# Kernel tuning notes

Measured on AMD Instinct MI355X. Metric: run time of the kernel, lower is better.

## Reference

```python
import jax, jax.numpy as jnp
import numpy as np

C_LIGHT = 3e8
SPATIAL, CROP = 128, 128
BIN_LEN, WALL_SIZE, SAMPLING_COEFF, CYCLES = 0.01, 2.0, 2.0, 5
B, D, T = 1, 2, 96


def waveconvparam(bin_resolution, virtual_wavelength, cycles):
    # Gaussian-windowed virtual cos/sin illumination wave (phasor-field heterodyne).
    s_z = bin_resolution * C_LIGHT
    samples = int(round(cycles * virtual_wavelength / s_z))
    num_cycles = samples * s_z / virtual_wavelength
    sigma = 0.3
    grids_k = np.arange(samples, dtype=np.float64) + 1.0
    sin_wave_k = np.sin(2.0 * np.pi * (num_cycles * grids_k) / samples)
    cos_wave_k = np.cos(2.0 * np.pi * (num_cycles * grids_k) / samples)
    n = np.arange(samples, dtype=np.float64) - (samples - 1) / 2.0
    window = np.exp(-0.5 * (n / (sigma * samples)) ** 2)
    return (cos_wave_k * window).astype(np.float32), (sin_wave_k * window).astype(np.float32)


def definePsf(sptial_grid, temprol_grid, slope):
    # Standard LCT light-cone PSF (O'Toole et al.).
    N, M = sptial_grid, temprol_grid
    x = np.linspace(-1.0, 1.0, 2 * N)
    y = np.linspace(-1.0, 1.0, 2 * N)
    z = np.linspace(0.0, 2.0, 2 * M)
    gz, gy, gx = np.meshgrid(z, y, x, indexing='ij')  # (2M, 2N, 2N)
    psf = np.abs(((4.0 * slope) ** 2) * (gx ** 2 + gy ** 2) - gz)
    psf = (psf == psf.min(axis=0, keepdims=True)).astype(np.float64)
    psf = psf / np.sum(psf[:, N, N])
    psf = psf / np.linalg.norm(psf.ravel())
    psf = np.roll(np.roll(psf, N, axis=1), N, axis=2)
    return psf


def resamplingOperator(M):
    mtx = np.zeros((M * M, M), dtype=np.float64)
    x = np.arange(1, M * M + 1)
    mtx[x - 1, np.ceil(np.sqrt(x)).astype(np.int64) - 1] = 1.0
    mtx = mtx / np.sqrt(x)[:, None]
    mtxi = mtx.T.copy()
    K = int(round(np.log2(M)))
    for _ in range(K):
        mtx = 0.5 * (mtx[0::2] + mtx[1::2])
        mtxi = 0.5 * (mtxi[:, 0::2] + mtxi[:, 1::2])
    return mtx.astype(np.float32), mtxi.astype(np.float32)


def setup_inputs() -> dict:
    key = jax.random.key(0)
    bin_resolution = BIN_LEN / C_LIGHT
    trange = CROP * C_LIGHT * bin_resolution
    width = WALL_SIZE / 2.0
    s_lamda_limit = WALL_SIZE / (SPATIAL - 1)
    virtual_wavelength = SAMPLING_COEFF * (s_lamda_limit * 2.0)
    cosw, sinw = waveconvparam(bin_resolution, virtual_wavelength, CYCLES)
    wave_2xk = np.stack([cosw, sinw], axis=0)[:, ::-1].copy()  # time-reversed, matches module
    psf = definePsf(SPATIAL, CROP, width / trange)
    invpsf = np.conjugate(np.fft.fftn(psf))  # (2*CROP, 2*SPATIAL, 2*SPATIAL)
    mtx, mtxi = resamplingOperator(CROP)
    feat = jax.random.normal(key, (B, D, T, SPATIAL, SPATIAL), dtype=jnp.float32)
    return {
        'feture_bxdxtxhxw': feat,
        'wave_2x1xk': jnp.asarray(wave_2xk[:, None, :], dtype=jnp.float32),
        'mtx_MxM': jnp.asarray(mtx),
        'mtxi_MxM': jnp.asarray(mtxi),
        'invpsf_real': jnp.asarray(np.real(invpsf).astype(np.float32)),
        'invpsf_imag': jnp.asarray(np.imag(invpsf).astype(np.float32)),
        'tbes': jnp.array([16], dtype=jnp.int32),
        'tens': jnp.array([112], dtype=jnp.int32),  # tens = tbes + T, used only via zero-padding
    }


def reference(feture_bxdxtxhxw, wave_2x1xk, mtx_MxM, mtxi_MxM, invpsf_real, invpsf_imag, tbes, tens):
    Bn, Dn, Tn, H, W = feture_bxdxtxhxw.shape
    M = mtx_MxM.shape[0]  # temporal grid (= crop)
    N = H                 # spatial grid
    BD = Bn * Dn

    # --- per-item zero-pad in time to length M (batched, replaces python loop) ---
    def pad_one(x_dthw, tbe):
        z = jnp.zeros((Dn, M, H, W), x_dthw.dtype)
        return jax.lax.dynamic_update_slice(z, x_dthw, (0, tbe, 0, 0))
    data = jax.vmap(pad_one)(feture_bxdxtxhxw, tbes).reshape(BD, M, H, W)

    # --- heterodyne: conv1d along time with reversed cos/sin virtual wave ---
    k = wave_2x1xk.shape[2]
    x = data.transpose(0, 2, 3, 1).reshape(BD * H * W, 1, M)
    y = jax.lax.conv_general_dilated(x, wave_2x1xk, (1,), [(k // 2, k // 2)],
                                     dimension_numbers=('NCH', 'OIH', 'NCH'))
    if k % 2 == 0:
        y = y[:, :, 1:]
    data2 = y.reshape(BD, H, W, 2, M).transpose(3, 0, 4, 1, 2).reshape(2 * BD, M, H, W)

    # --- resampling (LCT warp) ---
    tmp = jnp.einsum('mt,bthw->bmhw', mtx_MxM, data2)

    # --- batched 3D FFT deconvolution with conj(PSF spectrum) ---
    pad = jnp.zeros((2 * BD, 2 * M, 2 * N, 2 * N), tmp.dtype).at[:, :M, :N, :N].set(tmp)
    invpsf = invpsf_real + 1j * invpsf_imag  # complex64, (2M, 2N, 2N)
    vol = jnp.fft.ifftn(jnp.fft.fftn(pad, axes=(1, 2, 3)) * invpsf, axes=(1, 2, 3))[:, :M, :N, :N]

    # --- phasor magnitude: |cos_phasor^2 + sin_phasor^2| combine ---
    sq = vol[:BD] ** 2 + vol[BD:] ** 2  # Re = cr^2-ci^2+sr^2-si^2, Im = 2(cr*ci+sr*si)
    sum_real = jnp.real(sq)
    sum_imag = jnp.imag(sq)
    mag = jnp.sqrt(sum_real ** 2 + sum_imag ** 2)
    sqrt_sum = jnp.sqrt(jax.nn.relu((mag + sum_real) * 0.5))

    # --- inverse resampling ---
    out = jnp.einsum('mt,bthw->bmhw', mtxi_MxM, sqrt_sum)
    return out.reshape(Bn, Dn, M, H, W)
```

## Files before the change

### kernel.cpp

```cpp
#include <hip/hip_runtime.h>
#include <math.h>

typedef float2 c32;

__device__ __forceinline__ c32 cadd(c32 a, c32 b){ return make_float2(a.x+b.x, a.y+b.y); }
__device__ __forceinline__ c32 csub(c32 a, c32 b){ return make_float2(a.x-b.x, a.y-b.y); }
__device__ __forceinline__ c32 cmul(c32 a, c32 b){ return make_float2(fmaf(a.x,b.x,-a.y*b.y), fmaf(a.x,b.y,a.y*b.x)); }
__device__ __forceinline__ c32 cmulc(c32 a, c32 b){ return make_float2(fmaf(a.x,b.x, a.y*b.y), fmaf(a.y,b.x,-a.x*b.y)); }

__device__ __forceinline__ int dr4(int p){
  return ((p&3)<<6) | (((p>>2)&3)<<4) | (((p>>4)&3)<<2) | ((p>>6)&3);
}

template<int S>
__device__ __forceinline__ void dif16(c32 (&z)[16]){
  const float C1=0.92387953251128675613f, S1=0.38268343236508977173f, C2=0.70710678118654752440f;
  const float sg = (float)S;
  const c32 W[8] = { {1.f,0.f},{C1,sg*S1},{C2,sg*C2},{S1,sg*C1},{0.f,sg},{-S1,sg*C1},{-C2,sg*C2},{-C1,sg*S1} };
  #pragma unroll
  for(int j=0;j<8;j++){ c32 a=z[j], b=z[j+8]; z[j]=cadd(a,b); z[j+8]=cmul(csub(a,b), W[j]); }
  #pragma unroll
  for(int blk=0; blk<16; blk+=8){
    #pragma unroll
    for(int j=0;j<4;j++){ c32 a=z[blk+j], b=z[blk+j+4]; z[blk+j]=cadd(a,b); z[blk+j+4]=cmul(csub(a,b), W[2*j]); }
  }
  #pragma unroll
  for(int blk=0; blk<16; blk+=4){
    c32 a=z[blk], b=z[blk+2]; z[blk]=cadd(a,b); z[blk+2]=csub(a,b);
    c32 a1=z[blk+1], b1=z[blk+3]; c32 d=csub(a1,b1);
    z[blk+1]=cadd(a1,b1);
    z[blk+3]= (S<0)? make_float2(d.y,-d.x) : make_float2(-d.y,d.x);
  }
  #pragma unroll
  for(int blk=0; blk<16; blk+=2){ c32 a=z[blk], b=z[blk+1]; z[blk]=cadd(a,b); z[blk+1]=csub(a,b); }
}

__device__ __forceinline__ void dit16(c32 (&z)[16]){
  const float C1=0.92387953251128675613f, S1=0.38268343236508977173f, C2=0.70710678118654752440f;
  const c32 Wc[8] = { {1.f,0.f},{C1,S1},{C2,C2},{S1,C1},{0.f,1.f},{-S1,C1},{-C2,C2},{-C1,S1} };
  #pragma unroll
  for(int p=0;p<16;p+=2){ c32 a=z[p], b=z[p+1]; z[p]=cadd(a,b); z[p+1]=csub(a,b); }
  #pragma unroll
  for(int g=0;g<16;g+=4){
    c32 t=z[g+2]; z[g+2]=csub(z[g],t); z[g]=cadd(z[g],t);
    c32 u=z[g+3]; c32 t1=make_float2(-u.y,u.x); z[g+3]=csub(z[g+1],t1); z[g+1]=cadd(z[g+1],t1);
  }
  #pragma unroll
  for(int g=0;g<16;g+=8){
    #pragma unroll
    for(int j=0;j<4;j++){ c32 t=cmul(z[g+4+j], Wc[2*j]); z[g+4+j]=csub(z[g+j],t); z[g+j]=cadd(z[g+j],t); }
  }
  #pragma unroll
  for(int j=0;j<8;j++){ c32 t=cmul(z[8+j], Wc[j]); z[8+j]=csub(z[j],t); z[j]=cadd(z[j],t); }
}

__device__ __forceinline__ long magAddr(int d, int zz, int y, int x){
  int i = ((zz<<7) + y)*128 + x;
  int plane = i >> 15;
  int rem = i & 32767;
  return ((long)d<<24) + (long)plane*65536 + 32768 + rem;
}

__launch_bounds__(256)
__global__ void k_setup(const float* __restrict__ mtx, const float* __restrict__ wave,
                        const int* __restrict__ tbes, c32* __restrict__ A, c32* __restrict__ T,
                        int K, int P){
  __shared__ double2 w256[256];
  __shared__ double gre[128];
  __shared__ double gim[128];
  int tid=threadIdx.x; int v=blockIdx.x;
  double ang = -6.2831853071795864769252867665590 * (double)tid / 256.0;
  w256[tid]=make_double2(cos(ang), sin(ang));
  if(v==0) T[tid]=make_float2((float)w256[tid].x,(float)w256[tid].y);
  __syncthreads();
  if(tid<128){
    int tbe=tbes[0];
    double sr=0.0, si=0.0;
    for(int t=0;t<128;t++){
      int jj = v + tbe + P - t;
      if(jj>=0 && jj<K){
        double mv=(double)mtx[tid*128+t];
        sr += mv*(double)wave[jj];
        si += mv*(double)wave[K+jj];
      }
    }
    gre[tid]=sr; gim[tid]=si;
  }
  __syncthreads();
  double ar=0.0, ai=0.0;
  int k=tid;
  for(int m=0;m<128;m++){
    double2 f=w256[(k*m)&255];
    ar += f.x*gre[m] - f.y*gim[m];
    ai += f.x*gim[m] + f.y*gre[m];
  }
  A[(long)dr4(k)*96 + v] = make_float2((float)ar,(float)ai);
}

__launch_bounds__(256)
__global__ void k_front(const float* __restrict__ feat, const c32* __restrict__ A, c32* __restrict__ buf){
  __shared__ __align__(16) float Xs[48*128];
  __shared__ __align__(16) c32 As[64*48];
  int tid=threadIdx.x; int b=blockIdx.x;
  int d=b>>9, h=(b>>2)&127, kb=(b&3)*64;
  c32 acc[8][4];
  #pragma unroll
  for(int i=0;i<8;i++){
    #pragma unroll
    for(int j=0;j<4;j++) acc[i][j]=make_float2(0.f,0.f);
  }
  int kg=tid>>5, wg=tid&31;
  for(int vc=0; vc<2; vc++){
    #pragma unroll
    for(int i=0;i<6;i++){
      int idx=tid+i*256;
      int v=idx>>5, w4=idx&31;
      *(float4*)&Xs[v*128 + w4*4] = *(const float4*)&feat[(((long)d*96 + vc*48+v)*128 + h)*128 + w4*4];
    }
    #pragma unroll
    for(int i=0;i<6;i++){
      int idx=tid+i*256;
      int kk=idx/24, rem=idx-kk*24;
      *(float4*)&As[kk*48 + rem*2] = *(const float4*)&A[(long)(kb+kk)*96 + vc*48 + rem*2];
    }
    __syncthreads();
    #pragma unroll 4
    for(int vv=0; vv<48; vv++){
      float4 xv = *(const float4*)&Xs[vv*128 + wg*4];
      #pragma unroll
      for(int i=0;i<8;i++){
        c32 a = As[(kg*8+i)*48 + vv];
        acc[i][0].x = fmaf(a.x, xv.x, acc[i][0].x); acc[i][0].y = fmaf(a.y, xv.x, acc[i][0].y);
        acc[i][1].x = fmaf(a.x, xv.y, acc[i][1].x); acc[i][1].y = fmaf(a.y, xv.y, acc[i][1].y);
        acc[i][2].x = fmaf(a.x, xv.z, acc[i][2].x); acc[i][2].y = fmaf(a.y, xv.z, acc[i][2].y);
        acc[i][3].x = fmaf(a.x, xv.w, acc[i][3].x); acc[i][3].y = fmaf(a.y, xv.w, acc[i][3].y);
      }
    }
    __syncthreads();
  }
  #pragma unroll
  for(int i=0;i<8;i++){
    int k=kb+kg*8+i;
    long o = (((long)d*256 + k)*256 + h)*128 + wg*4;
    *(float4*)&buf[o]   = make_float4(acc[i][0].x,acc[i][0].y,acc[i][1].x,acc[i][1].y);
    *(float4*)&buf[o+2] = make_float4(acc[i][2].x,acc[i][2].y,acc[i][3].x,acc[i][3].y);
  }
}

__launch_bounds__(256)
__global__ void k_ffty(c32* __restrict__ buf, const c32* __restrict__ T){
  __shared__ c32 tile[256*17];
  __shared__ c32 Ts[256];
  int tid=threadIdx.x;
  Ts[tid]=T[tid];
  int b=blockIdx.x;
  int d=b>>11, k=(b>>3)&255, w0=(b&7)*16;
  long base = (((long)d*256 + k)*256)*128 + w0;
  __syncthreads();
  #pragma unroll
  for(int it=0; it<4; it++){
    int idx = tid + it*256; int w = idx&15, j = idx>>4;
    c32 x0 = buf[base + (long)j*128 + w];
    c32 x1 = buf[base + (long)(j+64)*128 + w];
    tile[j*17+w] = cadd(x0,x1);
    c32 y1 = make_float2(x0.x + x1.y, x0.y - x1.x);
    c32 y2 = csub(x0,x1);
    c32 y3 = make_float2(x0.x - x1.y, x0.y + x1.x);
    tile[(j+64)*17+w]  = cmul(y1, Ts[j]);
    tile[(j+128)*17+w] = cmul(y2, Ts[(2*j)&255]);
    tile[(j+192)*17+w] = cmul(y3, Ts[(3*j)&255]);
  }
  __syncthreads();
  #pragma unroll
  for(int s=1;s<4;s++){
    int quarter = 64 >> (2*s);
    int m4 = quarter<<2;
    int sh = 2*s;
    #pragma unroll
    for(int it=0;it<4;it++){
      int idx=tid+it*256; int w=idx&15, bf=idx>>4;
      int g = bf/quarter, j = bf - g*quarter;
      int p0 = g*m4 + j;
      c32 x0=tile[p0*17+w], x1=tile[(p0+quarter)*17+w], x2=tile[(p0+2*quarter)*17+w], x3=tile[(p0+3*quarter)*17+w];
      c32 t0=cadd(x0,x2), t1=csub(x0,x2), t2=cadd(x1,x3), t3=csub(x1,x3);
      c32 y0=cadd(t0,t2);
      c32 y2=csub(t0,t2);
      c32 y1=make_float2(t1.x + t3.y, t1.y - t3.x);
      c32 y3=make_float2(t1.x - t3.y, t1.y + t3.x);
      tile[p0*17+w]=y0;
      tile[(p0+quarter)*17+w]  =cmul(y1, Ts[(j<<sh)&255]);
      tile[(p0+2*quarter)*17+w]=cmul(y2, Ts[((2*j)<<sh)&255]);
      tile[(p0+3*quarter)*17+w]=cmul(y3, Ts[((3*j)<<sh)&255]);
    }
    __syncthreads();
  }
  #pragma unroll
  for(int it=0;it<16;it++){
    int idx=tid+it*256; int w=idx&15, p=idx>>4;
    buf[base + (long)p*128 + w] = tile[p*17+w];
  }
}

__launch_bounds__(256)
__global__ void k_fftx(c32* __restrict__ buf, const float* __restrict__ pre,
                       const float* __restrict__ pim, const c32* __restrict__ T){
  __shared__ float lre[16*272];
  __shared__ float lim[16*272];
  __shared__ c32 Ts[256];
  const int BR[16]={0,8,4,12,2,10,6,14,1,9,5,13,3,11,7,15};
  int tid=threadIdx.x;
  Ts[tid]=T[tid];
  int lane = tid & 63;
  int L = ((tid>>6)<<2) + (lane>>4);
  int n1 = lane & 15;
  int k = blockIdx.x >> 5;
  int q = ((blockIdx.x & 31)<<3) + (L & 7);
  int d = L >> 3;
  long lbase = (((long)d*256 + k)*256 + q)*128;
  int Lb = L*272;
  c32 z[16];
  #pragma unroll
  for(int r=0;r<8;r++) z[r] = buf[lbase + n1 + 16*r];
  #pragma unroll
  for(int r=8;r<16;r++) z[r] = make_float2(0.f,0.f);
  __syncthreads();
  dif16<-1>(z);
  #pragma unroll
  for(int r=1;r<16;r++) z[r] = cmul(z[r], Ts[(n1*BR[r])&255]);
  #pragma unroll
  for(int r=0;r<16;r++){ int o = Lb + BR[r]*17 + n1; lre[o]=z[r].x; lim[o]=z[r].y; }
  __syncthreads();
  #pragma unroll
  for(int c=0;c<16;c++){ int o = Lb + n1*17 + c; z[c]=make_float2(lre[o], lim[o]); }
  dif16<-1>(z);
  long prow = (((long)dr4(k))*256 + dr4(q))*256;
  #pragma unroll
  for(int r=0;r<16;r++){
    int kx = n1 + 16*BR[r];
    c32 h = make_float2(pre[prow+kx], pim[prow+kx]);
    z[r] = cmul(z[r], h);
  }
  dit16(z);
  #pragma unroll
  for(int r=1;r<16;r++) z[r] = cmulc(z[r], Ts[(r*n1)&255]);
  __syncthreads();
  #pragma unroll
  for(int r=0;r<16;r++){ int o = Lb + r*17 + n1; lre[o]=z[r].x; lim[o]=z[r].y; }
  __syncthreads();
  #pragma unroll
  for(int c=0;c<16;c++){ int o = Lb + n1*17 + c; z[c]=make_float2(lre[o], lim[o]); }
  dif16<1>(z);
  const float s = 1.f/256.f;
  #pragma unroll
  for(int r=0;r<16;r+=2){
    int n2 = BR[r];
    buf[lbase + n1 + 16*n2] = make_float2(z[r].x*s, z[r].y*s);
  }
}

__launch_bounds__(256)
__global__ void k_iffty(c32* __restrict__ buf, const c32* __restrict__ T){
  __shared__ c32 tile[256*17];
  __shared__ c32 Ts[256];
  int tid=threadIdx.x;
  Ts[tid]=T[tid];
  int b=blockIdx.x;
  int d=b>>11, k=(b>>3)&255, x0=(b&7)*16;
  long base = (((long)d*256 + k)*256)*128 + x0;
  __syncthreads();
  #pragma unroll
  for(int it=0;it<16;it++){
    int idx=tid+it*256; int w=idx&15, p=idx>>4;
    tile[p*17+w]=buf[base + (long)p*128 + w];
  }
  __syncthreads();
  #pragma unroll
  for(int s=0;s<3;s++){
    int quarter = 1<<(2*s);
    int m4 = quarter<<2;
    int sh = 2*(3-s);
    #pragma unroll
    for(int it=0;it<4;it++){
      int idx=tid+it*256; int w=idx&15, bf=idx>>4;
      int g=bf/quarter, j=bf-g*quarter;
      int p0=g*m4+j;
      c32 t0=tile[p0*17+w];
      c32 t1=cmulc(tile[(p0+quarter)*17+w],   Ts[(j<<sh)&255]);
      c32 t2=cmulc(tile[(p0+2*quarter)*17+w], Ts[((2*j)<<sh)&255]);
      c32 t3=cmulc(tile[(p0+3*quarter)*17+w], Ts[((3*j)<<sh)&255]);
      c32 y0 = make_float2(t0.x+t1.x+t2.x+t3.x, t0.y+t1.y+t2.y+t3.y);
      c32 y1 = make_float2(t0.x - t1.y - t2.x + t3.y, t0.y + t1.x - t2.y - t3.x);
      c32 y2 = make_float2(t0.x - t1.x + t2.x - t3.x, t0.y - t1.y + t2.y - t3.y);
      c32 y3 = make_float2(t0.x + t1.y - t2.x - t3.y, t0.y - t1.x - t2.y + t3.x);
      tile[p0*17+w]=y0; tile[(p0+quarter)*17+w]=y1; tile[(p0+2*quarter)*17+w]=y2; tile[(p0+3*quarter)*17+w]=y3;
    }
    __syncthreads();
  }
  const float sc = 1.f/256.f;
  #pragma unroll
  for(int it=0;it<4;it++){
    int idx=tid+it*256; int w=idx&15, j=idx>>4;
    c32 t0=tile[j*17+w];
    c32 t1=cmulc(tile[(j+64)*17+w],  Ts[j]);
    c32 t2=cmulc(tile[(j+128)*17+w], Ts[(2*j)&255]);
    c32 t3=cmulc(tile[(j+192)*17+w], Ts[(3*j)&255]);
    c32 y0 = make_float2((t0.x+t1.x+t2.x+t3.x)*sc, (t0.y+t1.y+t2.y+t3.y)*sc);
    c32 y1 = make_float2((t0.x - t1.y - t2.x + t3.y)*sc, (t0.y + t1.x - t2.y - t3.x)*sc);
    buf[base + (long)j*128 + w] = y0;
    buf[base + (long)(j+64)*128 + w] = y1;
  }
}

__launch_bounds__(256)
__global__ void k_ifftz(c32* __restrict__ buf, const c32* __restrict__ T){
  __shared__ c32 tile[256*17];
  __shared__ c32 Ts[256];
  float* magp = (float*)buf;
  int tid=threadIdx.x;
  Ts[tid]=T[tid];
  int b=blockIdx.x;
  int d=b>>10, y=(b>>3)&127, x0=(b&7)*16;
  __syncthreads();
  #pragma unroll
  for(int it=0;it<16;it++){
    int idx=tid+it*256; int w=idx&15, p=idx>>4;
    tile[p*17+w]=buf[(((long)d*256 + p)*256 + y)*128 + x0 + w];
  }
  __syncthreads();
  #pragma unroll
  for(int s=0;s<3;s++){
    int quarter = 1<<(2*s);
    int m4 = quarter<<2;
    int sh = 2*(3-s);
    #pragma unroll
    for(int it=0;it<4;it++){
      int idx=tid+it*256; int w=idx&15, bf=idx>>4;
      int g=bf/quarter, j=bf-g*quarter;
      int p0=g*m4+j;
      c32 t0=tile[p0*17+w];
      c32 t1=cmulc(tile[(p0+quarter)*17+w],   Ts[(j<<sh)&255]);
      c32 t2=cmulc(tile[(p0+2*quarter)*17+w], Ts[((2*j)<<sh)&255]);
      c32 t3=cmulc(tile[(p0+3*quarter)*17+w], Ts[((3*j)<<sh)&255]);
      c32 y0 = make_float2(t0.x+t1.x+t2.x+t3.x, t0.y+t1.y+t2.y+t3.y);
      c32 y1 = make_float2(t0.x - t1.y - t2.x + t3.y, t0.y + t1.x - t2.y - t3.x);
      c32 y2 = make_float2(t0.x - t1.x + t2.x - t3.x, t0.y - t1.y + t2.y - t3.y);
      c32 y3 = make_float2(t0.x + t1.y - t2.x - t3.y, t0.y - t1.x - t2.y + t3.x);
      tile[p0*17+w]=y0; tile[(p0+quarter)*17+w]=y1; tile[(p0+2*quarter)*17+w]=y2; tile[(p0+3*quarter)*17+w]=y3;
    }
    __syncthreads();
  }
  const float sc = 1.f/256.f;
  #pragma unroll
  for(int it=0;it<4;it++){
    int idx=tid+it*256; int w=idx&15, j=idx>>4;
    c32 t0=tile[j*17+w];
    c32 t1=cmulc(tile[(j+64)*17+w],  Ts[j]);
    c32 t2=cmulc(tile[(j+128)*17+w], Ts[(2*j)&255]);
    c32 t3=cmulc(tile[(j+192)*17+w], Ts[(3*j)&255]);
    float y0r = t0.x+t1.x+t2.x+t3.x, y0i = t0.y+t1.y+t2.y+t3.y;
    float y1r = t0.x - t1.y - t2.x + t3.y, y1i = t0.y + t1.x - t2.y - t3.x;
    magp[magAddr(d, j,    y, x0+w)] = sqrtf(y0r*y0r + y0i*y0i) * sc;
    magp[magAddr(d, j+64, y, x0+w)] = sqrtf(y1r*y1r + y1i*y1i) * sc;
  }
}

__launch_bounds__(256)
__global__ void k_post(const float* __restrict__ magp, const float* __restrict__ mtxi, float* __restrict__ out){
  __shared__ __align__(16) float magT[128*32];
  __shared__ __align__(16) float mt[128*70];
  int tid=threadIdx.x; int b=blockIdx.x;
  int d=b>>10, y=(b>>3)&127, x0=((b>>1)&3)*32, m0=(b&1)*64;
  #pragma unroll
  for(int it=0;it<16;it++){
    int idx=tid+it*256; int x=idx&31, t=idx>>5;
    magT[t*32+x] = magp[magAddr(d,t,y,x0+x)];
  }
  #pragma unroll
  for(int it=0;it<32;it++){
    int idx=tid+it*256; int mm=idx>>7, t=idx&127;
    mt[t*70+mm] = mtxi[(m0+mm)*128 + t];
  }
  __syncthreads();
  int xg=tid&7, mg=tid>>3;
  float4 a0=make_float4(0.f,0.f,0.f,0.f), a1=a0;
  #pragma unroll 4
  for(int t=0;t<128;t++){
    float2 mv = *(const float2*)&mt[t*70 + mg*2];
    float4 g  = *(const float4*)&magT[t*32 + xg*4];
    a0.x = fmaf(mv.x, g.x, a0.x); a0.y = fmaf(mv.x, g.y, a0.y);
    a0.z = fmaf(mv.x, g.z, a0.z); a0.w = fmaf(mv.x, g.w, a0.w);
    a1.x = fmaf(mv.y, g.x, a1.x); a1.y = fmaf(mv.y, g.y, a1.y);
    a1.z = fmaf(mv.y, g.z, a1.z); a1.w = fmaf(mv.y, g.w, a1.w);
  }
  int m_ = m0 + mg*2;
  *(float4*)&out[(((long)d*128 + m_  )*128 + y)*128 + x0 + xg*4] = a0;
  *(float4*)&out[(((long)d*128 + m_+1)*128 + y)*128 + x0 + xg*4] = a1;
}

extern "C" void kernel_launch(void* const* d_in, const int* in_sizes, int n_in,
                              void* d_out, int out_size, void* d_ws, size_t ws_size,
                              hipStream_t stream) {
  const float* feat=(const float*)d_in[0];
  const float* wave=(const float*)d_in[1];
  const float* mtx =(const float*)d_in[2];
  const float* mtxi=(const float*)d_in[3];
  const float* pre =(const float*)d_in[4];
  const float* pim =(const float*)d_in[5];
  const int*   tbes=(const int*)d_in[6];
  float* out=(float*)d_out;
  char* ws=(char*)d_ws;
  c32* A   = (c32*)ws;
  c32* T   = (c32*)(ws + 196608);
  c32* buf = (c32*)(ws + 262144);

  int K = in_sizes[1] / 2;
  int P = (K & 1) ? (K/2) : (K/2 - 1);

  hipLaunchKernelGGL(k_setup, dim3(96),   dim3(256), 0, stream, mtx, wave, tbes, A, T, K, P);
  hipLaunchKernelGGL(k_front, dim3(1024), dim3(256), 0, stream, feat, A, buf);
  hipLaunchKernelGGL(k_ffty,  dim3(4096), dim3(256), 0, stream, buf, T);
  hipLaunchKernelGGL(k_fftx,  dim3(8192), dim3(256), 0, stream, buf, pre, pim, T);
  hipLaunchKernelGGL(k_iffty, dim3(4096), dim3(256), 0, stream, buf, T);
  hipLaunchKernelGGL(k_ifftz, dim3(2048), dim3(256), 0, stream, buf, T);
  hipLaunchKernelGGL(k_post,  dim3(2048), dim3(256), 0, stream, (const float*)buf, mtxi, out);
}
```

Before: 247.1 us.

## Fuse y-FFT, x-FFT with PSF multiply, and inverse y-FFT into one plane kernel

Three separate kernels (forward y-FFT, x-FFT with PSF multiply and inverse x-FFT, inverse y-FFT) are replaced by one k_plane kernel. Each 1024-thread block holds a whole (d,k) plane in shared memory and runs the 256-point y transform as 16x8x2 stages, with the zero-padded half split into two passes (py). The x transforms do their transpose with warp shuffles instead of LDS round trips. This removes two full global-memory round trips of the large complex buffer and two launches. In exchange, the kernel uses about 132KB of shared memory, runs 512 large blocks with low occupancy, and needs more register pressure and syncthreads.

```diff
diff --git a/kernel.cpp b/kernel.cpp
--- a/kernel.cpp
+++ b/kernel.cpp
@@ -52,6 +52,48 @@
   }
   #pragma unroll
   for(int j=0;j<8;j++){ c32 t=cmul(z[8+j], Wc[j]); z[8+j]=csub(z[j],t); z[j]=cadd(z[j],t); }
+}
+
+template<int S>
+__device__ __forceinline__ void dif8(c32 (&z)[8]){
+  const float C2=0.70710678118654752440f;
+  const float sg=(float)S;
+  const c32 W1=make_float2(C2, sg*C2), W2=make_float2(0.f,sg), W3=make_float2(-C2, sg*C2);
+  {
+    c32 a0=z[0],a1=z[1],a2=z[2],a3=z[3],b0=z[4],b1=z[5],b2=z[6],b3=z[7];
+    z[0]=cadd(a0,b0); z[4]=csub(a0,b0);
+    z[1]=cadd(a1,b1); z[5]=cmul(csub(a1,b1),W1);
+    z[2]=cadd(a2,b2); z[6]=cmul(csub(a2,b2),W2);
+    z[3]=cadd(a3,b3); z[7]=cmul(csub(a3,b3),W3);
+  }
+  #pragma unroll
+  for(int h=0;h<8;h+=4){
+    c32 a0=z[h],a1=z[h+1],b0=z[h+2],b1=z[h+3];
+    z[h]=cadd(a0,b0); z[h+2]=csub(a0,b0);
+    c32 dd=csub(a1,b1); z[h+1]=cadd(a1,b1);
+    z[h+3]= (S<0)? make_float2(dd.y,-dd.x) : make_float2(-dd.y,dd.x);
+  }
+  #pragma unroll
+  for(int p=0;p<8;p+=2){ c32 a=z[p],b=z[p+1]; z[p]=cadd(a,b); z[p+1]=csub(a,b); }
+}
+
+__device__ __forceinline__ void transpose16(c32 (&z)[16], int lane){
+  #pragma unroll
+  for(int bsh=0; bsh<4; bsh++){
+    const int b = 1<<bsh;
+    c32 t[16];
+    #pragma unroll
+    for(int r=0;r<16;r++){
+      t[r].x = __shfl_xor(z[r^b].x, b, 16);
+      t[r].y = __shfl_xor(z[r^b].y, b, 16);
+    }
+    #pragma unroll
+    for(int r=0;r<16;r++){
+      bool keep = ((lane & b) == (r & b));
+      z[r].x = keep ? z[r].x : t[r].x;
+      z[r].y = keep ? z[r].y : t[r].y;
+    }
+  }
 }
 
 __device__ __forceinline__ long magAddr(int d, int zz, int y, int x){
@@ -147,167 +189,137 @@
   }
 }
 
-__launch_bounds__(256)
-__global__ void k_ffty(c32* __restrict__ buf, const c32* __restrict__ T){
-  __shared__ c32 tile[256*17];
-  __shared__ c32 Ts[256];
-  int tid=threadIdx.x;
-  Ts[tid]=T[tid];
-  int b=blockIdx.x;
-  int d=b>>11, k=(b>>3)&255, w0=(b&7)*16;
-  long base = (((long)d*256 + k)*256)*128 + w0;
-  __syncthreads();
-  #pragma unroll
-  for(int it=0; it<4; it++){
-    int idx = tid + it*256; int w = idx&15, j = idx>>4;
-    c32 x0 = buf[base + (long)j*128 + w];
-    c32 x1 = buf[base + (long)(j+64)*128 + w];
-    tile[j*17+w] = cadd(x0,x1);
-    c32 y1 = make_float2(x0.x + x1.y, x0.y - x1.x);
-    c32 y2 = csub(x0,x1);
-    c32 y3 = make_float2(x0.x - x1.y, x0.y + x1.x);
-    tile[(j+64)*17+w]  = cmul(y1, Ts[j]);
-    tile[(j+128)*17+w] = cmul(y2, Ts[(2*j)&255]);
-    tile[(j+192)*17+w] = cmul(y3, Ts[(3*j)&255]);
-  }
-  __syncthreads();
-  #pragma unroll
-  for(int s=1;s<4;s++){
-    int quarter = 64 >> (2*s);
-    int m4 = quarter<<2;
-    int sh = 2*s;
-    #pragma unroll
-    for(int it=0;it<4;it++){
-      int idx=tid+it*256; int w=idx&15, bf=idx>>4;
-      int g = bf/quarter, j = bf - g*quarter;
-      int p0 = g*m4 + j;
-      c32 x0=tile[p0*17+w], x1=tile[(p0+quarter)*17+w], x2=tile[(p0+2*quarter)*17+w], x3=tile[(p0+3*quarter)*17+w];
-      c32 t0=cadd(x0,x2), t1=csub(x0,x2), t2=cadd(x1,x3), t3=csub(x1,x3);
-      c32 y0=cadd(t0,t2);
-      c32 y2=csub(t0,t2);
-      c32 y1=make_float2(t1.x + t3.y, t1.y - t3.x);
-      c32 y3=make_float2(t1.x - t3.y, t1.y + t3.x);
-      tile[p0*17+w]=y0;
-      tile[(p0+quarter)*17+w]  =cmul(y1, Ts[(j<<sh)&255]);
-      tile[(p0+2*quarter)*17+w]=cmul(y2, Ts[((2*j)<<sh)&255]);
-      tile[(p0+3*quarter)*17+w]=cmul(y3, Ts[((3*j)<<sh)&255]);
-    }
-    __syncthreads();
-  }
-  #pragma unroll
-  for(int it=0;it<16;it++){
-    int idx=tid+it*256; int w=idx&15, p=idx>>4;
-    buf[base + (long)p*128 + w] = tile[p*17+w];
-  }
-}
-
-__launch_bounds__(256)
-__global__ void k_fftx(c32* __restrict__ buf, const float* __restrict__ pre,
-                       const float* __restrict__ pim, const c32* __restrict__ T){
-  __shared__ float lre[16*272];
-  __shared__ float lim[16*272];
+#define PSTR 129
+__launch_bounds__(1024)
+__global__ void k_plane(c32* __restrict__ buf, const float* __restrict__ pre,
+                        const float* __restrict__ pim, const c32* __restrict__ T){
+  __shared__ float Pre[128*PSTR];
+  __shared__ float Pim[128*PSTR];
   __shared__ c32 Ts[256];
   const int BR[16]={0,8,4,12,2,10,6,14,1,9,5,13,3,11,7,15};
+  const int BR3[8]={0,4,2,6,1,5,3,7};
   int tid=threadIdx.x;
-  Ts[tid]=T[tid];
-  int lane = tid & 63;
-  int L = ((tid>>6)<<2) + (lane>>4);
-  int n1 = lane & 15;
-  int k = blockIdx.x >> 5;
-  int q = ((blockIdx.x & 31)<<3) + (L & 7);
-  int d = L >> 3;
-  long lbase = (((long)d*256 + k)*256 + q)*128;
-  int Lb = L*272;
-  c32 z[16];
-  #pragma unroll
-  for(int r=0;r<8;r++) z[r] = buf[lbase + n1 + 16*r];
-  #pragma unroll
-  for(int r=8;r<16;r++) z[r] = make_float2(0.f,0.f);
-  __syncthreads();
-  dif16<-1>(z);
-  #pragma unroll
-  for(int r=1;r<16;r++) z[r] = cmul(z[r], Ts[(n1*BR[r])&255]);
-  #pragma unroll
-  for(int r=0;r<16;r++){ int o = Lb + BR[r]*17 + n1; lre[o]=z[r].x; lim[o]=z[r].y; }
-  __syncthreads();
-  #pragma unroll
-  for(int c=0;c<16;c++){ int o = Lb + n1*17 + c; z[c]=make_float2(lre[o], lim[o]); }
-  dif16<-1>(z);
-  long prow = (((long)dr4(k))*256 + dr4(q))*256;
-  #pragma unroll
-  for(int r=0;r<16;r++){
-    int kx = n1 + 16*BR[r];
-    c32 h = make_float2(pre[prow+kx], pim[prow+kx]);
-    z[r] = cmul(z[r], h);
-  }
-  dit16(z);
-  #pragma unroll
-  for(int r=1;r<16;r++) z[r] = cmulc(z[r], Ts[(r*n1)&255]);
-  __syncthreads();
-  #pragma unroll
-  for(int r=0;r<16;r++){ int o = Lb + r*17 + n1; lre[o]=z[r].x; lim[o]=z[r].y; }
-  __syncthreads();
-  #pragma unroll
-  for(int c=0;c<16;c++){ int o = Lb + n1*17 + c; z[c]=make_float2(lre[o], lim[o]); }
-  dif16<1>(z);
-  const float s = 1.f/256.f;
-  #pragma unroll
-  for(int r=0;r<16;r+=2){
-    int n2 = BR[r];
-    buf[lbase + n1 + 16*n2] = make_float2(z[r].x*s, z[r].y*s);
-  }
-}
-
-__launch_bounds__(256)
-__global__ void k_iffty(c32* __restrict__ buf, const c32* __restrict__ T){
-  __shared__ c32 tile[256*17];
-  __shared__ c32 Ts[256];
-  int tid=threadIdx.x;
-  Ts[tid]=T[tid];
-  int b=blockIdx.x;
-  int d=b>>11, k=(b>>3)&255, x0=(b&7)*16;
-  long base = (((long)d*256 + k)*256)*128 + x0;
-  __syncthreads();
-  #pragma unroll
-  for(int it=0;it<16;it++){
-    int idx=tid+it*256; int w=idx&15, p=idx>>4;
-    tile[p*17+w]=buf[base + (long)p*128 + w];
-  }
-  __syncthreads();
-  #pragma unroll
-  for(int s=0;s<3;s++){
-    int quarter = 1<<(2*s);
-    int m4 = quarter<<2;
-    int sh = 2*(3-s);
-    #pragma unroll
-    for(int it=0;it<4;it++){
-      int idx=tid+it*256; int w=idx&15, bf=idx>>4;
-      int g=bf/quarter, j=bf-g*quarter;
-      int p0=g*m4+j;
-      c32 t0=tile[p0*17+w];
-      c32 t1=cmulc(tile[(p0+quarter)*17+w],   Ts[(j<<sh)&255]);
-      c32 t2=cmulc(tile[(p0+2*quarter)*17+w], Ts[((2*j)<<sh)&255]);
-      c32 t3=cmulc(tile[(p0+3*quarter)*17+w], Ts[((3*j)<<sh)&255]);
-      c32 y0 = make_float2(t0.x+t1.x+t2.x+t3.x, t0.y+t1.y+t2.y+t3.y);
-      c32 y1 = make_float2(t0.x - t1.y - t2.x + t3.y, t0.y + t1.x - t2.y - t3.x);
-      c32 y2 = make_float2(t0.x - t1.x + t2.x - t3.x, t0.y - t1.y + t2.y - t3.y);
-      c32 y3 = make_float2(t0.x + t1.y - t2.x - t3.y, t0.y - t1.x - t2.y + t3.x);
-      tile[p0*17+w]=y0; tile[(p0+quarter)*17+w]=y1; tile[(p0+2*quarter)*17+w]=y2; tile[(p0+3*quarter)*17+w]=y3;
-    }
-    __syncthreads();
-  }
-  const float sc = 1.f/256.f;
-  #pragma unroll
-  for(int it=0;it<4;it++){
-    int idx=tid+it*256; int w=idx&15, j=idx>>4;
-    c32 t0=tile[j*17+w];
-    c32 t1=cmulc(tile[(j+64)*17+w],  Ts[j]);
-    c32 t2=cmulc(tile[(j+128)*17+w], Ts[(2*j)&255]);
-    c32 t3=cmulc(tile[(j+192)*17+w], Ts[(3*j)&255]);
-    c32 y0 = make_float2((t0.x+t1.x+t2.x+t3.x)*sc, (t0.y+t1.y+t2.y+t3.y)*sc);
-    c32 y1 = make_float2((t0.x - t1.y - t2.x + t3.y)*sc, (t0.y + t1.x - t2.y - t3.x)*sc);
-    buf[base + (long)j*128 + w] = y0;
-    buf[base + (long)(j+64)*128 + w] = y1;
+  if(tid<256) Ts[tid]=T[tid];
+  int b=blockIdx.x; int d=b>>8, k=b&255;
+  long pbase = (((long)d*256 + k)*256)*128;
+  int g = tid>>7, x = tid&127;
+  int lane16 = tid&15, rowslot = tid>>4;
+  long prowz = ((long)dr4(k))*65536;
+  c32 Oacc[16];
+  #pragma unroll
+  for(int j=0;j<16;j++) Oacc[j]=make_float2(0.f,0.f);
+
+  for(int py=0; py<2; py++){
+    c32 v[16];
+    #pragma unroll
+    for(int j=0;j<16;j++){
+      c32 val = buf[pbase + (long)(g+8*j)*128 + x];
+      if(py){ val = cmul(val, Ts[g+8*j]); }
+      v[j]=val;
+    }
+    __syncthreads();
+    dif16<-1>(v);
+    #pragma unroll
+    for(int r=0;r<16;r++){
+      int k1 = BR[r];
+      c32 val = cmul(v[r], Ts[(2*g*k1)&255]);
+      int row = k1*8+g;
+      Pre[row*PSTR+x]=val.x; Pim[row*PSTR+x]=val.y;
+    }
+    __syncthreads();
+    c32 u0[8], u1[8];
+    #pragma unroll
+    for(int gp=0; gp<8; gp++){
+      int r0=(2*g)*8+gp;
+      u0[gp]=make_float2(Pre[r0*PSTR+x],Pim[r0*PSTR+x]);
+      u1[gp]=make_float2(Pre[(r0+8)*PSTR+x],Pim[(r0+8)*PSTR+x]);
+    }
+    __syncthreads();
+    dif8<-1>(u0); dif8<-1>(u1);
+    #pragma unroll
+    for(int r=0;r<8;r++){
+      int row0=2*g+16*BR3[r];
+      Pre[row0*PSTR+x]=u0[r].x;     Pim[row0*PSTR+x]=u0[r].y;
+      Pre[(row0+1)*PSTR+x]=u1[r].x; Pim[(row0+1)*PSTR+x]=u1[r].y;
+    }
+    __syncthreads();
+    #pragma unroll
+    for(int s=0;s<2;s++){
+      int row = s*64 + rowslot;
+      long prow = prowz + (long)(2*row+py)*256;
+      c32 z[16];
+      #pragma unroll
+      for(int r=0;r<8;r++) z[r]=make_float2(Pre[row*PSTR + lane16 + 16*r], Pim[row*PSTR + lane16 + 16*r]);
+      #pragma unroll
+      for(int r=8;r<16;r++) z[r]=make_float2(0.f,0.f);
+      dif16<-1>(z);
+      #pragma unroll
+      for(int r=1;r<16;r++) z[r]=cmul(z[r], Ts[(lane16*BR[r])&255]);
+      c32 y[16];
+      #pragma unroll
+      for(int a=0;a<16;a++) y[a]=z[BR[a]];
+      transpose16(y, lane16);
+      dif16<-1>(y);
+      #pragma unroll
+      for(int r=0;r<16;r++){
+        int kx = lane16 + 16*BR[r];
+        c32 h = make_float2(pre[prow+kx], pim[prow+kx]);
+        y[r]=cmul(y[r],h);
+      }
+      dit16(y);
+      #pragma unroll
+      for(int r=1;r<16;r++) y[r]=cmulc(y[r], Ts[(r*lane16)&255]);
+      transpose16(y, lane16);
+      dif16<1>(y);
+      const float s256=1.f/256.f;
+      #pragma unroll
+      for(int r=0;r<16;r+=2){
+        int n2=BR[r];
+        Pre[row*PSTR + lane16 + 16*n2] = y[r].x*s256;
+        Pim[row*PSTR + lane16 + 16*n2] = y[r].y*s256;
+      }
+    }
+    __syncthreads();
+    c32 R0[8], R1[8];
+    #pragma unroll
+    for(int k2=0;k2<8;k2++){
+      int row0=2*g+16*k2;
+      R0[k2]=make_float2(Pre[row0*PSTR+x],Pim[row0*PSTR+x]);
+      R1[k2]=make_float2(Pre[(row0+1)*PSTR+x],Pim[(row0+1)*PSTR+x]);
+    }
+    __syncthreads();
+    dif8<1>(R0); dif8<1>(R1);
+    #pragma unroll
+    for(int r=0;r<8;r++){
+      int q8=BR3[r];
+      Pre[(q8*16+2*g)*PSTR+x]=R0[r].x;   Pim[(q8*16+2*g)*PSTR+x]=R0[r].y;
+      Pre[(q8*16+2*g+1)*PSTR+x]=R1[r].x; Pim[(q8*16+2*g+1)*PSTR+x]=R1[r].y;
+    }
+    __syncthreads();
+    c32 w[16];
+    #pragma unroll
+    for(int k1=0;k1<16;k1++){
+      c32 val=make_float2(Pre[(g*16+k1)*PSTR+x],Pim[(g*16+k1)*PSTR+x]);
+      w[k1]=cmulc(val, Ts[(2*g*k1)&255]);
+    }
+    dif16<1>(w);
+    const float sy=1.f/256.f;
+    #pragma unroll
+    for(int j=0;j<16;j++){
+      int q=g+8*j;
+      c32 val=w[BR[j]];
+      if(py==0){
+        Oacc[j].x += val.x*sy; Oacc[j].y += val.y*sy;
+      } else {
+        c32 tw=Ts[q];
+        Oacc[j].x += (val.x*tw.x + val.y*tw.y)*sy;
+        Oacc[j].y += (val.y*tw.x - val.x*tw.y)*sy;
+      }
+    }
+  }
+  #pragma unroll
+  for(int j=0;j<16;j++){
+    buf[pbase + (long)(g+8*j)*128 + x] = Oacc[j];
   }
 }
 
@@ -416,11 +428,9 @@
   int K = in_sizes[1] / 2;
   int P = (K & 1) ? (K/2) : (K/2 - 1);
 
-  hipLaunchKernelGGL(k_setup, dim3(96),   dim3(256), 0, stream, mtx, wave, tbes, A, T, K, P);
-  hipLaunchKernelGGL(k_front, dim3(1024), dim3(256), 0, stream, feat, A, buf);
-  hipLaunchKernelGGL(k_ffty,  dim3(4096), dim3(256), 0, stream, buf, T);
-  hipLaunchKernelGGL(k_fftx,  dim3(8192), dim3(256), 0, stream, buf, pre, pim, T);
-  hipLaunchKernelGGL(k_iffty, dim3(4096), dim3(256), 0, stream, buf, T);
-  hipLaunchKernelGGL(k_ifftz, dim3(2048), dim3(256), 0, stream, buf, T);
-  hipLaunchKernelGGL(k_post,  dim3(2048), dim3(256), 0, stream, (const float*)buf, mtxi, out);
-}
+  hipLaunchKernelGGL(k_setup, dim3(96),   dim3(256),  0, stream, mtx, wave, tbes, A, T, K, P);
+  hipLaunchKernelGGL(k_front, dim3(1024), dim3(256),  0, stream, feat, A, buf);
+  hipLaunchKernelGGL(k_plane, dim3(512),  dim3(1024), 0, stream, buf, pre, pim, T);
+  hipLaunchKernelGGL(k_ifftz, dim3(2048), dim3(256),  0, stream, buf, T);
+  hipLaunchKernelGGL(k_post,  dim3(2048), dim3(256),  0, stream, (const float*)buf, mtxi, out);
+}
```

New measurement: 528.0 us. 114% more time.

## Fuse inverse z-FFT with inverse resampling and use wave barriers in x-FFT

Applied to the files above, without the earlier changes.

Merges the inverse z-FFT and inverse-resampling matmul into one kernel. Each block keeps its 128x16 magnitude tile in shared memory instead of writing it to global memory and reading it back in a separate launch. The x-FFT kernel now uses an interleaved complex shared tile and wave-level barriers in place of block-wide syncs, since each 16-thread group only exchanges data within its own wavefront. The cost is that each block reloads the full mtxi matrix in two halves, and the post stage runs with a narrower per-block x tile.

```diff
diff --git a/kernel.cpp b/kernel.cpp
--- a/kernel.cpp
+++ b/kernel.cpp
@@ -52,13 +52,6 @@
   }
   #pragma unroll
   for(int j=0;j<8;j++){ c32 t=cmul(z[8+j], Wc[j]); z[8+j]=csub(z[j],t); z[j]=cadd(z[j],t); }
-}
-
-__device__ __forceinline__ long magAddr(int d, int zz, int y, int x){
-  int i = ((zz<<7) + y)*128 + x;
-  int plane = i >> 15;
-  int rem = i & 32767;
-  return ((long)d<<24) + (long)plane*65536 + 32768 + rem;
 }
 
 __launch_bounds__(256)
@@ -204,8 +197,7 @@
 __launch_bounds__(256)
 __global__ void k_fftx(c32* __restrict__ buf, const float* __restrict__ pre,
                        const float* __restrict__ pim, const c32* __restrict__ T){
-  __shared__ float lre[16*272];
-  __shared__ float lim[16*272];
+  __shared__ c32 tile[16*276];
   __shared__ c32 Ts[256];
   const int BR[16]={0,8,4,12,2,10,6,14,1,9,5,13,3,11,7,15};
   int tid=threadIdx.x;
@@ -217,7 +209,7 @@
   int q = ((blockIdx.x & 31)<<3) + (L & 7);
   int d = L >> 3;
   long lbase = (((long)d*256 + k)*256 + q)*128;
-  int Lb = L*272;
+  c32* tl = &tile[L*276];
   c32 z[16];
   #pragma unroll
   for(int r=0;r<8;r++) z[r] = buf[lbase + n1 + 16*r];
@@ -228,10 +220,10 @@
   #pragma unroll
   for(int r=1;r<16;r++) z[r] = cmul(z[r], Ts[(n1*BR[r])&255]);
   #pragma unroll
-  for(int r=0;r<16;r++){ int o = Lb + BR[r]*17 + n1; lre[o]=z[r].x; lim[o]=z[r].y; }
-  __syncthreads();
-  #pragma unroll
-  for(int c=0;c<16;c++){ int o = Lb + n1*17 + c; z[c]=make_float2(lre[o], lim[o]); }
+  for(int r=0;r<16;r++) tl[BR[r]*17 + n1] = z[r];
+  __builtin_amdgcn_wave_barrier();
+  #pragma unroll
+  for(int c=0;c<16;c++) z[c] = tl[n1*17 + c];
   dif16<-1>(z);
   long prow = (((long)dr4(k))*256 + dr4(q))*256;
   #pragma unroll
@@ -243,12 +235,12 @@
   dit16(z);
   #pragma unroll
   for(int r=1;r<16;r++) z[r] = cmulc(z[r], Ts[(r*n1)&255]);
-  __syncthreads();
-  #pragma unroll
-  for(int r=0;r<16;r++){ int o = Lb + r*17 + n1; lre[o]=z[r].x; lim[o]=z[r].y; }
-  __syncthreads();
-  #pragma unroll
-  for(int c=0;c<16;c++){ int o = Lb + n1*17 + c; z[c]=make_float2(lre[o], lim[o]); }
+  __builtin_amdgcn_wave_barrier();
+  #pragma unroll
+  for(int r=0;r<16;r++) tl[r*17 + n1] = z[r];
+  __builtin_amdgcn_wave_barrier();
+  #pragma unroll
+  for(int c=0;c<16;c++) z[c] = tl[n1*17 + c];
   dif16<1>(z);
   const float s = 1.f/256.f;
   #pragma unroll
@@ -312,10 +304,11 @@
 }
 
 __launch_bounds__(256)
-__global__ void k_ifftz(c32* __restrict__ buf, const c32* __restrict__ T){
+__global__ void k_back(c32* __restrict__ buf, const float* __restrict__ mtxi,
+                       const c32* __restrict__ T, float* __restrict__ out){
   __shared__ c32 tile[256*17];
+  __shared__ float magl[128*16];
   __shared__ c32 Ts[256];
-  float* magp = (float*)buf;
   int tid=threadIdx.x;
   Ts[tid]=T[tid];
   int b=blockIdx.x;
@@ -359,42 +352,32 @@
     c32 t3=cmulc(tile[(j+192)*17+w], Ts[(3*j)&255]);
     float y0r = t0.x+t1.x+t2.x+t3.x, y0i = t0.y+t1.y+t2.y+t3.y;
     float y1r = t0.x - t1.y - t2.x + t3.y, y1i = t0.y + t1.x - t2.y - t3.x;
-    magp[magAddr(d, j,    y, x0+w)] = sqrtf(y0r*y0r + y0i*y0i) * sc;
-    magp[magAddr(d, j+64, y, x0+w)] = sqrtf(y1r*y1r + y1i*y1i) * sc;
-  }
-}
-
-__launch_bounds__(256)
-__global__ void k_post(const float* __restrict__ magp, const float* __restrict__ mtxi, float* __restrict__ out){
-  __shared__ __align__(16) float magT[128*32];
-  __shared__ __align__(16) float mt[128*70];
-  int tid=threadIdx.x; int b=blockIdx.x;
-  int d=b>>10, y=(b>>3)&127, x0=((b>>1)&3)*32, m0=(b&1)*64;
-  #pragma unroll
-  for(int it=0;it<16;it++){
-    int idx=tid+it*256; int x=idx&31, t=idx>>5;
-    magT[t*32+x] = magp[magAddr(d,t,y,x0+x)];
-  }
-  #pragma unroll
-  for(int it=0;it<32;it++){
-    int idx=tid+it*256; int mm=idx>>7, t=idx&127;
-    mt[t*70+mm] = mtxi[(m0+mm)*128 + t];
-  }
-  __syncthreads();
-  int xg=tid&7, mg=tid>>3;
-  float4 a0=make_float4(0.f,0.f,0.f,0.f), a1=a0;
-  #pragma unroll 4
-  for(int t=0;t<128;t++){
-    float2 mv = *(const float2*)&mt[t*70 + mg*2];
-    float4 g  = *(const float4*)&magT[t*32 + xg*4];
-    a0.x = fmaf(mv.x, g.x, a0.x); a0.y = fmaf(mv.x, g.y, a0.y);
-    a0.z = fmaf(mv.x, g.z, a0.z); a0.w = fmaf(mv.x, g.w, a0.w);
-    a1.x = fmaf(mv.y, g.x, a1.x); a1.y = fmaf(mv.y, g.y, a1.y);
-    a1.z = fmaf(mv.y, g.z, a1.z); a1.w = fmaf(mv.y, g.w, a1.w);
-  }
-  int m_ = m0 + mg*2;
-  *(float4*)&out[(((long)d*128 + m_  )*128 + y)*128 + x0 + xg*4] = a0;
-  *(float4*)&out[(((long)d*128 + m_+1)*128 + y)*128 + x0 + xg*4] = a1;
+    magl[j*16 + w]      = sqrtf(y0r*y0r + y0i*y0i) * sc;
+    magl[(j+64)*16 + w] = sqrtf(y1r*y1r + y1i*y1i) * sc;
+  }
+  __syncthreads();
+  float* mt = (float*)tile;
+  int xg = tid&3, mg = tid>>2;
+  #pragma unroll
+  for(int c=0;c<2;c++){
+    #pragma unroll
+    for(int it=0;it<32;it++){
+      int idx=tid+it*256; int t=idx&127, mm=idx>>7;
+      mt[t*68+mm] = mtxi[(c*64+mm)*128 + t];
+    }
+    __syncthreads();
+    float4 a = make_float4(0.f,0.f,0.f,0.f);
+    #pragma unroll 4
+    for(int t=0;t<128;t++){
+      float mv = mt[t*68 + mg];
+      float4 g = *(const float4*)&magl[t*16 + xg*4];
+      a.x = fmaf(mv, g.x, a.x); a.y = fmaf(mv, g.y, a.y);
+      a.z = fmaf(mv, g.z, a.z); a.w = fmaf(mv, g.w, a.w);
+    }
+    int m_ = c*64 + mg;
+    *(float4*)&out[(((long)d*128 + m_)*128 + y)*128 + x0 + xg*4] = a;
+    __syncthreads();
+  }
 }
 
 extern "C" void kernel_launch(void* const* d_in, const int* in_sizes, int n_in,
@@ -421,6 +404,5 @@
   hipLaunchKernelGGL(k_ffty,  dim3(4096), dim3(256), 0, stream, buf, T);
   hipLaunchKernelGGL(k_fftx,  dim3(8192), dim3(256), 0, stream, buf, pre, pim, T);
   hipLaunchKernelGGL(k_iffty, dim3(4096), dim3(256), 0, stream, buf, T);
-  hipLaunchKernelGGL(k_ifftz, dim3(2048), dim3(256), 0, stream, buf, T);
-  hipLaunchKernelGGL(k_post,  dim3(2048), dim3(256), 0, stream, (const float*)buf, mtxi, out);
-}
+  hipLaunchKernelGGL(k_back,  dim3(2048), dim3(256), 0, stream, buf, mtxi, T, out);
+}
```

New measurement: 252.7 us. 2.3% more time.
